# Kernel tuning notes

Measured on AMD Instinct MI355X. Metric: run time of the kernel, lower is better.

## Reference

```python
import jax, jax.numpy as jnp
import numpy as np

OUT_H = 7
OUT_W = 7
SPATIAL_SCALE = 0.25


def setup_inputs() -> dict:
    key = jax.random.key(0)
    k1, k2, k3, k4 = jax.random.split(key, 4)
    B, C, H, W = 2, 256, 256, 256
    N = 512  # rois per image
    x = jax.random.normal(k1, (B, C, H, W), dtype=jnp.float32)
    cxy = jax.random.uniform(k2, (B, N, 2), minval=0.0, maxval=1024.0, dtype=jnp.float32)
    wh = jax.random.uniform(k3, (B, N, 2), minval=16.0, maxval=256.0, dtype=jnp.float32)
    ang = jax.random.uniform(k4, (B, N, 1), minval=-90.0, maxval=90.0, dtype=jnp.float32)
    boxes = jnp.concatenate([cxy, wh, ang], axis=-1)  # [B, N, 5] = (cx, cy, w, h, angle_deg)
    return {"x": x, "boxes": boxes}


def _rroi_pool(feat, rois):
    # feat: [B, C, H, W]; rois: [R, 6] = (batch_idx, cx, cy, w, h, angle_deg)
    B, C, H, W = feat.shape
    R = rois.shape[0]
    b_idx = rois[:, 0].astype(jnp.int32)
    cx = rois[:, 1] * SPATIAL_SCALE
    cy = rois[:, 2] * SPATIAL_SCALE
    w = rois[:, 3] * SPATIAL_SCALE
    h = rois[:, 4] * SPATIAL_SCALE
    ang = rois[:, 5] * (jnp.pi / 180.0)
    # affine transform from bin-grid coords to (scaled) image coords (RRPN kernel)
    dx = -OUT_W / 2.0
    dy = -OUT_H / 2.0
    Sx = w / OUT_W
    Sy = h / OUT_H
    ca = jnp.cos(ang)
    sa = jnp.sin(ang)
    M00 = ca * Sx
    M01 = sa * Sy
    M02 = ca * Sx * dx + sa * Sy * dy + cx
    M10 = -sa * Sx
    M11 = ca * Sy
    M12 = -sa * Sx * dx + ca * Sy * dy + cy

    ph, pw = jnp.meshgrid(jnp.arange(OUT_H, dtype=jnp.float32),
                          jnp.arange(OUT_W, dtype=jnp.float32), indexing='ij')
    # 4 corners of each bin: offsets in (pw, ph)
    offs = jnp.array([[0.0, 0.0], [0.0, 1.0], [1.0, 0.0], [1.0, 1.0]], dtype=jnp.float32)
    pw_c = pw[None] + offs[:, 0][:, None, None]  # [4, OH, OW]
    ph_c = ph[None] + offs[:, 1][:, None, None]

    def aff(m0, m1, m2):
        # [R,1,1,1] * [4,OH,OW] -> [R,4,OH,OW]
        return (m0[:, None, None, None] * pw_c[None]
                + m1[:, None, None, None] * ph_c[None]
                + m2[:, None, None, None])

    Xc = aff(M00, M01, M02)  # x coords of bin corners
    Yc = aff(M10, M11, M12)
    leftMost = jnp.maximum(jnp.round(Xc.min(axis=1)), 0.0)            # [R,OH,OW]
    rightMost = jnp.minimum(jnp.round(Xc.max(axis=1)), W - 1.0)
    topMost = jnp.maximum(jnp.round(Yc.min(axis=1)), 0.0)
    bottomMost = jnp.minimum(jnp.round(Yc.max(axis=1)), H - 1.0)

    bin_cx = (leftMost + rightMost) / 2.0
    bin_cy = (topMost + bottomMost) / 2.0
    bin_l = jnp.floor(bin_cx).astype(jnp.int32)
    bin_r = jnp.ceil(bin_cx).astype(jnp.int32)
    bin_t = jnp.floor(bin_cy).astype(jnp.int32)
    bin_b = jnp.ceil(bin_cy).astype(jnp.int32)
    rx = bin_cx - jnp.floor(bin_cx)
    ry = bin_cy - jnp.floor(bin_cy)

    feat_t = feat.transpose(0, 2, 3, 1)  # [B, H, W, C]
    bi = b_idx[:, None, None]            # [R,1,1]

    def gather(yi, xi):
        valid = (yi >= 0) & (yi < H) & (xi >= 0) & (xi < W)
        yc = jnp.clip(yi, 0, H - 1)
        xc = jnp.clip(xi, 0, W - 1)
        v = feat_t[bi, yc, xc]                      # [R, OH, OW, C]
        return jnp.where(valid[..., None], v, 0.0)

    lt = gather(bin_t, bin_l)
    rt = gather(bin_t, bin_r)
    lb = gather(bin_b, bin_l)
    rb = gather(bin_b, bin_r)

    wlt = ((1.0 - rx) * (1.0 - ry))[..., None]
    wrt = (rx * (1.0 - ry))[..., None]
    wrb = (rx * ry)[..., None]
    wlb = ((1.0 - rx) * ry)[..., None]

    inter = lt * wlt + rt * wrt + rb * wrb + lb * wlb  # [R, OH, OW, C]
    out = jnp.maximum(inter, 0.0)  # kernel inits maxval=0 before the single sample
    return out.transpose(0, 3, 1, 2)  # [R, C, OH, OW]


def reference(x, boxes):
    # x: [B, C, H, W]; boxes: [B, N, 5]
    B, N = boxes.shape[0], boxes.shape[1]
    ids = jnp.repeat(jnp.arange(B, dtype=boxes.dtype), N)[:, None]  # convert_to_roi_format
    rois = jnp.concatenate([ids, boxes.reshape(B * N, 5)], axis=1)  # [R, 6]
    return _rroi_pool(x, rois)
```

## Files before the change

kernel.cpp:

```cpp
#include <hip/hip_runtime.h>

#define NBINS 49
#define NCH   256
#define FH    256
#define FW    256
#define HWSZ  (FH * FW)

typedef float f4 __attribute__((ext_vector_type(4)));

#define TD 64
__global__ __launch_bounds__(256) void transpose_chw_hwc(
    const float* __restrict__ in,
    float* __restrict__ outT)
{
    __shared__ float tile[TD][TD + 1];
    const int t   = threadIdx.x;
    const int hw0 = blockIdx.x * TD;
    const int c0  = blockIdx.y * TD;
    const int bz  = blockIdx.z;
    const float* A = in   + (size_t)bz * NCH * HWSZ;
    float*       B = outT + (size_t)bz * HWSZ * NCH;

    const int hwq = (t & 15) * 4;
    const int cr  = t >> 4;
    #pragma unroll
    for (int k = 0; k < 4; ++k) {
        int c = cr + k * 16;
        f4 v = __builtin_nontemporal_load(
                   (const f4*)&A[(size_t)(c0 + c) * HWSZ + hw0 + hwq]);
        tile[c][hwq + 0] = v.x;
        tile[c][hwq + 1] = v.y;
        tile[c][hwq + 2] = v.z;
        tile[c][hwq + 3] = v.w;
    }
    __syncthreads();
    const int cq  = (t & 15) * 4;
    const int hwr = t >> 4;
    #pragma unroll
    for (int k = 0; k < 4; ++k) {
        int hw = hwr + k * 16;
        f4 v;
        v.x = tile[cq + 0][hw];
        v.y = tile[cq + 1][hw];
        v.z = tile[cq + 2][hw];
        v.w = tile[cq + 3][hw];
        *(f4*)&B[(size_t)(hw0 + hw) * NCH + c0 + cq] = v;
    }
}

__global__ __launch_bounds__(256, 4) void rroi_pool_nhwc(
    const float* __restrict__ xt,
    const float* __restrict__ boxes,
    float* __restrict__ out)
{
    __shared__ int   s_oTL[NBINS], s_oTR[NBINS], s_oBL[NBINS], s_oBR[NBINS];
    __shared__ float s_wlt[NBINS], s_wrt[NBINS], s_wrb[NBINS], s_wlb[NBINS];
    __shared__ __align__(16) float s_stage[128 * NBINS];

    const int roi = blockIdx.x;
    const int tid = threadIdx.x;
    const int b   = roi >> 9;

    if (tid < NBINS) {
        const float* bx = boxes + roi * 5;
        float cx  = __fmul_rn(bx[0], 0.25f);
        float cy  = __fmul_rn(bx[1], 0.25f);
        float w   = __fmul_rn(bx[2], 0.25f);
        float h   = __fmul_rn(bx[3], 0.25f);
        float ang = __fmul_rn(bx[4], 0.017453292519943295f);
        float ca = (float)cos((double)ang);
        float sa = (float)sin((double)ang);
        float Sx = __fdiv_rn(w, 7.0f);
        float Sy = __fdiv_rn(h, 7.0f);
        const float dx = -3.5f, dy = -3.5f;
        float M00 = __fmul_rn(ca, Sx);
        float M01 = __fmul_rn(sa, Sy);
        float M02 = __fadd_rn(__fadd_rn(__fmul_rn(M00, dx), __fmul_rn(M01, dy)), cx);
        float nsa = -sa;
        float M10 = __fmul_rn(nsa, Sx);
        float M11 = __fmul_rn(ca, Sy);
        float M12 = __fadd_rn(__fadd_rn(__fmul_rn(M10, dx), __fmul_rn(M11, dy)), cy);

        int ph = tid / 7, pw = tid % 7;
        float minX = 1e30f, maxX = -1e30f, minY = 1e30f, maxY = -1e30f;
        #pragma unroll
        for (int o0 = 0; o0 < 2; ++o0) {
            #pragma unroll
            for (int o1 = 0; o1 < 2; ++o1) {
                float px = (float)(pw + o0);
                float py = (float)(ph + o1);
                float Xc = __fadd_rn(__fadd_rn(__fmul_rn(M00, px), __fmul_rn(M01, py)), M02);
                float Yc = __fadd_rn(__fadd_rn(__fmul_rn(M10, px), __fmul_rn(M11, py)), M12);
                minX = fminf(minX, Xc); maxX = fmaxf(maxX, Xc);
                minY = fminf(minY, Yc); maxY = fmaxf(maxY, Yc);
            }
        }
        float leftMost   = fmaxf(rintf(minX), 0.0f);
        float rightMost  = fminf(rintf(maxX), (float)(FW - 1));
        float topMost    = fmaxf(rintf(minY), 0.0f);
        float bottomMost = fminf(rintf(maxY), (float)(FH - 1));
        float bcx = __fmul_rn(__fadd_rn(leftMost, rightMost), 0.5f);
        float bcy = __fmul_rn(__fadd_rn(topMost, bottomMost), 0.5f);
        float fl = floorf(bcx), ft = floorf(bcy);
        int l   = (int)fl;
        int r   = (int)ceilf(bcx);
        int t   = (int)ft;
        int btm = (int)ceilf(bcy);
        float rx = __fsub_rn(bcx, fl);
        float ry = __fsub_rn(bcy, ft);

        bool vl = (unsigned)l   < (unsigned)FW;
        bool vr = (unsigned)r   < (unsigned)FW;
        bool vt = (unsigned)t   < (unsigned)FH;
        bool vb = (unsigned)btm < (unsigned)FH;
        int xl = min(max(l, 0), FW - 1), xr = min(max(r, 0), FW - 1);
        int yt = min(max(t, 0), FH - 1), yb = min(max(btm, 0), FH - 1);

        s_oTL[tid] = yt * FW + xl;
        s_oTR[tid] = yt * FW + xr;
        s_oBL[tid] = yb * FW + xl;
        s_oBR[tid] = yb * FW + xr;
        float w_lt = (1.0f - rx) * (1.0f - ry);
        float w_rt = rx * (1.0f - ry);
        float w_rb = rx * ry;
        float w_lb = (1.0f - rx) * ry;
        s_wlt[tid] = (vt && vl) ? w_lt : 0.0f;
        s_wrt[tid] = (vt && vr) ? w_rt : 0.0f;
        s_wrb[tid] = (vb && vr) ? w_rb : 0.0f;
        s_wlb[tid] = (vb && vl) ? w_lb : 0.0f;
    }
    __syncthreads();

    const float* fb = xt + (size_t)b * HWSZ * NCH;
    float p[NBINS];
    #pragma unroll
    for (int bin = 0; bin < NBINS; ++bin) {
        int oTL = __builtin_amdgcn_readfirstlane(s_oTL[bin]);
        int oTR = __builtin_amdgcn_readfirstlane(s_oTR[bin]);
        int oBL = __builtin_amdgcn_readfirstlane(s_oBL[bin]);
        int oBR = __builtin_amdgcn_readfirstlane(s_oBR[bin]);
        float wlt = s_wlt[bin], wrt = s_wrt[bin], wrb = s_wrb[bin], wlb = s_wlb[bin];
        float lt = fb[(size_t)oTL * NCH + tid];
        float rt = fb[(size_t)oTR * NCH + tid];
        float lb = fb[(size_t)oBL * NCH + tid];
        float rb = fb[(size_t)oBR * NCH + tid];
        float v = lt * wlt + rt * wrt + rb * wrb + lb * wlb;
        p[bin] = fmaxf(v, 0.0f);
    }

    f4* out4 = (f4*)(out + (size_t)roi * NCH * NBINS);
    const f4* lds4 = (const f4*)s_stage;
    const int HV4 = 128 * NBINS / 4;
    #pragma unroll
    for (int half = 0; half < 2; ++half) {
        __syncthreads();
        if ((tid >> 7) == half) {
            float* dst = s_stage + (tid & 127) * NBINS;
            #pragma unroll
            for (int bin = 0; bin < NBINS; ++bin) dst[bin] = p[bin];
        }
        __syncthreads();
        for (int j = tid; j < HV4; j += 256)
            __builtin_nontemporal_store(lds4[j], &out4[half * HV4 + j]);
    }
}

__global__ __launch_bounds__(256) void rroi_pool_chw(
    const float* __restrict__ x, const float* __restrict__ boxes, float* __restrict__ out)
{
    __shared__ int   s_l[NBINS], s_r[NBINS], s_t[NBINS], s_b[NBINS];
    __shared__ float s_rx[NBINS], s_ry[NBINS];
    const int roi = blockIdx.x, tid = threadIdx.x, b = roi >> 9;
    if (tid < NBINS) {
        const float* bx = boxes + roi * 5;
        float cx  = __fmul_rn(bx[0], 0.25f);
        float cy  = __fmul_rn(bx[1], 0.25f);
        float w   = __fmul_rn(bx[2], 0.25f);
        float h   = __fmul_rn(bx[3], 0.25f);
        float ang = __fmul_rn(bx[4], 0.017453292519943295f);
        float ca = (float)cos((double)ang);
        float sa = (float)sin((double)ang);
        float Sx = __fdiv_rn(w, 7.0f);
        float Sy = __fdiv_rn(h, 7.0f);
        const float dx = -3.5f, dy = -3.5f;
        float M00 = __fmul_rn(ca, Sx);
        float M01 = __fmul_rn(sa, Sy);
        float M02 = __fadd_rn(__fadd_rn(__fmul_rn(M00, dx), __fmul_rn(M01, dy)), cx);
        float nsa = -sa;
        float M10 = __fmul_rn(nsa, Sx);
        float M11 = __fmul_rn(ca, Sy);
        float M12 = __fadd_rn(__fadd_rn(__fmul_rn(M10, dx), __fmul_rn(M11, dy)), cy);
        int ph = tid / 7, pw = tid % 7;
        float minX = 1e30f, maxX = -1e30f, minY = 1e30f, maxY = -1e30f;
        #pragma unroll
        for (int o0 = 0; o0 < 2; ++o0)
            #pragma unroll
            for (int o1 = 0; o1 < 2; ++o1) {
                float px = (float)(pw + o0);
                float py = (float)(ph + o1);
                float Xc = __fadd_rn(__fadd_rn(__fmul_rn(M00, px), __fmul_rn(M01, py)), M02);
                float Yc = __fadd_rn(__fadd_rn(__fmul_rn(M10, px), __fmul_rn(M11, py)), M12);
                minX = fminf(minX, Xc); maxX = fmaxf(maxX, Xc);
                minY = fminf(minY, Yc); maxY = fmaxf(maxY, Yc);
            }
        float leftMost   = fmaxf(rintf(minX), 0.0f);
        float rightMost  = fminf(rintf(maxX), (float)(FW - 1));
        float topMost    = fmaxf(rintf(minY), 0.0f);
        float bottomMost = fminf(rintf(maxY), (float)(FH - 1));
        float bcx = __fmul_rn(__fadd_rn(leftMost, rightMost), 0.5f);
        float bcy = __fmul_rn(__fadd_rn(topMost, bottomMost), 0.5f);
        float fl = floorf(bcx), ft = floorf(bcy);
        s_l[tid] = (int)fl;  s_r[tid] = (int)ceilf(bcx);
        s_t[tid] = (int)ft;  s_b[tid] = (int)ceilf(bcy);
        s_rx[tid] = __fsub_rn(bcx, fl);
        s_ry[tid] = __fsub_rn(bcy, ft);
    }
    __syncthreads();
    const float* featb = x + (size_t)b * NCH * HWSZ;
    float* outr = out + (size_t)roi * NCH * NBINS;
    for (int i = tid; i < NCH * NBINS; i += 256) {
        int c = i / NBINS, bin = i - c * NBINS;
        int l = s_l[bin], r = s_r[bin], t = s_t[bin], btm = s_b[bin];
        float rx = s_rx[bin], ry = s_ry[bin];
        const float* fc = featb + (size_t)c * HWSZ;
        bool vl = (unsigned)l < (unsigned)FW, vr = (unsigned)r < (unsigned)FW;
        bool vt = (unsigned)t < (unsigned)FH, vb = (unsigned)btm < (unsigned)FH;
        int lc = min(max(l, 0), FW - 1), rc = min(max(r, 0), FW - 1);
        int tc = min(max(t, 0), FH - 1), bc = min(max(btm, 0), FH - 1);
        float lt = (vt && vl) ? fc[tc * FW + lc] : 0.0f;
        float rt = (vt && vr) ? fc[tc * FW + rc] : 0.0f;
        float lb = (vb && vl) ? fc[bc * FW + lc] : 0.0f;
        float rb = (vb && vr) ? fc[bc * FW + rc] : 0.0f;
        float w_lt = (1.0f - rx) * (1.0f - ry);
        float w_rt = rx * (1.0f - ry);
        float w_rb = rx * ry;
        float w_lb = (1.0f - rx) * ry;
        float v = lt * w_lt + rt * w_rt + rb * w_rb + lb * w_lb;
        outr[i] = fmaxf(v, 0.0f);
    }
}

extern "C" void kernel_launch(void* const* d_in, const int* in_sizes, int n_in,
                              void* d_out, int out_size, void* d_ws, size_t ws_size,
                              hipStream_t stream) {
    const float* x     = (const float*)d_in[0];
    const float* boxes = (const float*)d_in[1];
    float* out = (float*)d_out;
    (void)in_sizes; (void)n_in; (void)out_size;

    const size_t need = (size_t)2 * NCH * HWSZ * sizeof(float);
    if (ws_size >= need) {
        float* xt = (float*)d_ws;
        transpose_chw_hwc<<<dim3(HWSZ / TD, NCH / TD, 2), dim3(256), 0, stream>>>(x, xt);
        rroi_pool_nhwc<<<dim3(1024), dim3(256), 0, stream>>>(xt, boxes, out);
    } else {
        rroi_pool_chw<<<dim3(1024), dim3(256), 0, stream>>>(x, boxes, out);
    }
}
```

Measured before the change: 70.96 us.

## Transpose only feature pixels referenced by ROI bins via occupancy bitmap

Adds a pre-pass kernel that computes each ROI's bin sample corners and atomically sets bits in a per-batch pixel-occupancy bitmap. The CHW→HWC transpose then skips 64-pixel tiles with no referenced pixels and writes only the pixel rows that are marked. The goal is to cut the write traffic of the large transposed workspace, and part of the read traffic. The cost is an extra memset, a small bitmap kernel and its atomics, and duplicated bin geometry math.

After: 93.80 us. +32.2%, slower.

```diff
diff --git a/kernel.cpp b/kernel.cpp
--- a/kernel.cpp
+++ b/kernel.cpp
@@ -5,19 +5,116 @@
 #define FH    256
 #define FW    256
 #define HWSZ  (FH * FW)
+#define BMWORDS 2048
 
 typedef float f4 __attribute__((ext_vector_type(4)));
+
+__device__ __forceinline__ void bin_geom(const float* __restrict__ bx, int tid,
+                                         int& oTL, int& oTR, int& oBL, int& oBR,
+                                         float& wlt, float& wrt, float& wrb, float& wlb)
+{
+    float cx  = __fmul_rn(bx[0], 0.25f);
+    float cy  = __fmul_rn(bx[1], 0.25f);
+    float w   = __fmul_rn(bx[2], 0.25f);
+    float h   = __fmul_rn(bx[3], 0.25f);
+    float ang = __fmul_rn(bx[4], 0.017453292519943295f);
+    float ca = (float)cos((double)ang);
+    float sa = (float)sin((double)ang);
+    float Sx = __fdiv_rn(w, 7.0f);
+    float Sy = __fdiv_rn(h, 7.0f);
+    const float dx = -3.5f, dy = -3.5f;
+    float M00 = __fmul_rn(ca, Sx);
+    float M01 = __fmul_rn(sa, Sy);
+    float M02 = __fadd_rn(__fadd_rn(__fmul_rn(M00, dx), __fmul_rn(M01, dy)), cx);
+    float nsa = -sa;
+    float M10 = __fmul_rn(nsa, Sx);
+    float M11 = __fmul_rn(ca, Sy);
+    float M12 = __fadd_rn(__fadd_rn(__fmul_rn(M10, dx), __fmul_rn(M11, dy)), cy);
+
+    int ph = tid / 7, pw = tid % 7;
+    float minX = 1e30f, maxX = -1e30f, minY = 1e30f, maxY = -1e30f;
+    #pragma unroll
+    for (int o0 = 0; o0 < 2; ++o0) {
+        #pragma unroll
+        for (int o1 = 0; o1 < 2; ++o1) {
+            float px = (float)(pw + o0);
+            float py = (float)(ph + o1);
+            float Xc = __fadd_rn(__fadd_rn(__fmul_rn(M00, px), __fmul_rn(M01, py)), M02);
+            float Yc = __fadd_rn(__fadd_rn(__fmul_rn(M10, px), __fmul_rn(M11, py)), M12);
+            minX = fminf(minX, Xc); maxX = fmaxf(maxX, Xc);
+            minY = fminf(minY, Yc); maxY = fmaxf(maxY, Yc);
+        }
+    }
+    float leftMost   = fmaxf(rintf(minX), 0.0f);
+    float rightMost  = fminf(rintf(maxX), (float)(FW - 1));
+    float topMost    = fmaxf(rintf(minY), 0.0f);
+    float bottomMost = fminf(rintf(maxY), (float)(FH - 1));
+    float bcx = __fmul_rn(__fadd_rn(leftMost, rightMost), 0.5f);
+    float bcy = __fmul_rn(__fadd_rn(topMost, bottomMost), 0.5f);
+    float fl = floorf(bcx), ft = floorf(bcy);
+    int l   = (int)fl;
+    int r   = (int)ceilf(bcx);
+    int t   = (int)ft;
+    int btm = (int)ceilf(bcy);
+    float rx = __fsub_rn(bcx, fl);
+    float ry = __fsub_rn(bcy, ft);
+
+    bool vl = (unsigned)l   < (unsigned)FW;
+    bool vr = (unsigned)r   < (unsigned)FW;
+    bool vt = (unsigned)t   < (unsigned)FH;
+    bool vb = (unsigned)btm < (unsigned)FH;
+    int xl = min(max(l, 0), FW - 1), xr = min(max(r, 0), FW - 1);
+    int yt = min(max(t, 0), FH - 1), yb = min(max(btm, 0), FH - 1);
+
+    oTL = yt * FW + xl;
+    oTR = yt * FW + xr;
+    oBL = yb * FW + xl;
+    oBR = yb * FW + xr;
+    float w_lt = (1.0f - rx) * (1.0f - ry);
+    float w_rt = rx * (1.0f - ry);
+    float w_rb = rx * ry;
+    float w_lb = (1.0f - rx) * ry;
+    wlt = (vt && vl) ? w_lt : 0.0f;
+    wrt = (vt && vr) ? w_rt : 0.0f;
+    wrb = (vb && vr) ? w_rb : 0.0f;
+    wlb = (vb && vl) ? w_lb : 0.0f;
+}
+
+__global__ __launch_bounds__(64) void build_bitmap(
+    const float* __restrict__ boxes,
+    unsigned long long* __restrict__ bm)
+{
+    const int roi = blockIdx.x;
+    const int tid = threadIdx.x;
+    if (tid >= NBINS) return;
+    const int b = roi >> 9;
+    int oTL, oTR, oBL, oBR; float wlt, wrt, wrb, wlb;
+    bin_geom(boxes + roi * 5, tid, oTL, oTR, oBL, oBR, wlt, wrt, wrb, wlb);
+    unsigned long long* base = bm + (size_t)b * 1024;
+    atomicOr(&base[oTL >> 6], 1ull << (oTL & 63));
+    atomicOr(&base[oTR >> 6], 1ull << (oTR & 63));
+    atomicOr(&base[oBL >> 6], 1ull << (oBL & 63));
+    atomicOr(&base[oBR >> 6], 1ull << (oBR & 63));
+}
 
 #define TD 64
 __global__ __launch_bounds__(256) void transpose_chw_hwc(
     const float* __restrict__ in,
-    float* __restrict__ outT)
+    float* __restrict__ outT,
+    const unsigned long long* __restrict__ bm)
 {
     __shared__ float tile[TD][TD + 1];
     const int t   = threadIdx.x;
     const int hw0 = blockIdx.x * TD;
     const int c0  = blockIdx.y * TD;
     const int bz  = blockIdx.z;
+
+    unsigned long long mask = ~0ull;
+    if (bm) {
+        mask = bm[(size_t)bz * 1024 + blockIdx.x];
+        if (mask == 0ull) return;
+    }
+
     const float* A = in   + (size_t)bz * NCH * HWSZ;
     float*       B = outT + (size_t)bz * HWSZ * NCH;
 
@@ -39,12 +136,14 @@
     #pragma unroll
     for (int k = 0; k < 4; ++k) {
         int hw = hwr + k * 16;
-        f4 v;
-        v.x = tile[cq + 0][hw];
-        v.y = tile[cq + 1][hw];
-        v.z = tile[cq + 2][hw];
-        v.w = tile[cq + 3][hw];
-        *(f4*)&B[(size_t)(hw0 + hw) * NCH + c0 + cq] = v;
+        if ((mask >> hw) & 1ull) {
+            f4 v;
+            v.x = tile[cq + 0][hw];
+            v.y = tile[cq + 1][hw];
+            v.z = tile[cq + 2][hw];
+            v.w = tile[cq + 3][hw];
+            *(f4*)&B[(size_t)(hw0 + hw) * NCH + c0 + cq] = v;
+        }
     }
 }
 
@@ -62,72 +161,12 @@
     const int b   = roi >> 9;
 
     if (tid < NBINS) {
-        const float* bx = boxes + roi * 5;
-        float cx  = __fmul_rn(bx[0], 0.25f);
-        float cy  = __fmul_rn(bx[1], 0.25f);
-        float w   = __fmul_rn(bx[2], 0.25f);
-        float h   = __fmul_rn(bx[3], 0.25f);
-        float ang = __fmul_rn(bx[4], 0.017453292519943295f);
-        float ca = (float)cos((double)ang);
-        float sa = (float)sin((double)ang);
-        float Sx = __fdiv_rn(w, 7.0f);
-        float Sy = __fdiv_rn(h, 7.0f);
-        const float dx = -3.5f, dy = -3.5f;
-        float M00 = __fmul_rn(ca, Sx);
-        float M01 = __fmul_rn(sa, Sy);
-        float M02 = __fadd_rn(__fadd_rn(__fmul_rn(M00, dx), __fmul_rn(M01, dy)), cx);
-        float nsa = -sa;
-        float M10 = __fmul_rn(nsa, Sx);
-        float M11 = __fmul_rn(ca, Sy);
-        float M12 = __fadd_rn(__fadd_rn(__fmul_rn(M10, dx), __fmul_rn(M11, dy)), cy);
-
-        int ph = tid / 7, pw = tid % 7;
-        float minX = 1e30f, maxX = -1e30f, minY = 1e30f, maxY = -1e30f;
-        #pragma unroll
-        for (int o0 = 0; o0 < 2; ++o0) {
-            #pragma unroll
-            for (int o1 = 0; o1 < 2; ++o1) {
-                float px = (float)(pw + o0);
-                float py = (float)(ph + o1);
-                float Xc = __fadd_rn(__fadd_rn(__fmul_rn(M00, px), __fmul_rn(M01, py)), M02);
-                float Yc = __fadd_rn(__fadd_rn(__fmul_rn(M10, px), __fmul_rn(M11, py)), M12);
-                minX = fminf(minX, Xc); maxX = fmaxf(maxX, Xc);
-                minY = fminf(minY, Yc); maxY = fmaxf(maxY, Yc);
-            }
-        }
-        float leftMost   = fmaxf(rintf(minX), 0.0f);
-        float rightMost  = fminf(rintf(maxX), (float)(FW - 1));
-        float topMost    = fmaxf(rintf(minY), 0.0f);
-        float bottomMost = fminf(rintf(maxY), (float)(FH - 1));
-        float bcx = __fmul_rn(__fadd_rn(leftMost, rightMost), 0.5f);
-        float bcy = __fmul_rn(__fadd_rn(topMost, bottomMost), 0.5f);
-        float fl = floorf(bcx), ft = floorf(bcy);
-        int l   = (int)fl;
-        int r   = (int)ceilf(bcx);
-        int t   = (int)ft;
-        int btm = (int)ceilf(bcy);
-        float rx = __fsub_rn(bcx, fl);
-        float ry = __fsub_rn(bcy, ft);
-
-        bool vl = (unsigned)l   < (unsigned)FW;
-        bool vr = (unsigned)r   < (unsigned)FW;
-        bool vt = (unsigned)t   < (unsigned)FH;
-        bool vb = (unsigned)btm < (unsigned)FH;
-        int xl = min(max(l, 0), FW - 1), xr = min(max(r, 0), FW - 1);
-        int yt = min(max(t, 0), FH - 1), yb = min(max(btm, 0), FH - 1);
-
-        s_oTL[tid] = yt * FW + xl;
-        s_oTR[tid] = yt * FW + xr;
-        s_oBL[tid] = yb * FW + xl;
-        s_oBR[tid] = yb * FW + xr;
-        float w_lt = (1.0f - rx) * (1.0f - ry);
-        float w_rt = rx * (1.0f - ry);
-        float w_rb = rx * ry;
-        float w_lb = (1.0f - rx) * ry;
-        s_wlt[tid] = (vt && vl) ? w_lt : 0.0f;
-        s_wrt[tid] = (vt && vr) ? w_rt : 0.0f;
-        s_wrb[tid] = (vb && vr) ? w_rb : 0.0f;
-        s_wlb[tid] = (vb && vl) ? w_lb : 0.0f;
+        int oTL, oTR, oBL, oBR; float wlt, wrt, wrb, wlb;
+        bin_geom(boxes + roi * 5, tid, oTL, oTR, oBL, oBR, wlt, wrt, wrb, wlb);
+        s_oTL[tid] = oTL;  s_oTR[tid] = oTR;
+        s_oBL[tid] = oBL;  s_oBR[tid] = oBR;
+        s_wlt[tid] = wlt;  s_wrt[tid] = wrt;
+        s_wrb[tid] = wrb;  s_wlb[tid] = wlb;
     }
     __syncthreads();
 
@@ -248,10 +287,19 @@
     float* out = (float*)d_out;
     (void)in_sizes; (void)n_in; (void)out_size;
 
-    const size_t need = (size_t)2 * NCH * HWSZ * sizeof(float);
-    if (ws_size >= need) {
+    const size_t need_xt = (size_t)2 * NCH * HWSZ * sizeof(float);
+    const size_t need_bm = need_xt + BMWORDS * sizeof(unsigned long long);
+
+    if (ws_size >= need_bm) {
         float* xt = (float*)d_ws;
-        transpose_chw_hwc<<<dim3(HWSZ / TD, NCH / TD, 2), dim3(256), 0, stream>>>(x, xt);
+        unsigned long long* bm = (unsigned long long*)((char*)d_ws + need_xt);
+        hipMemsetAsync(bm, 0, BMWORDS * sizeof(unsigned long long), stream);
+        build_bitmap<<<dim3(1024), dim3(64), 0, stream>>>(boxes, bm);
+        transpose_chw_hwc<<<dim3(HWSZ / TD, NCH / TD, 2), dim3(256), 0, stream>>>(x, xt, bm);
+        rroi_pool_nhwc<<<dim3(1024), dim3(256), 0, stream>>>(xt, boxes, out);
+    } else if (ws_size >= need_xt) {
+        float* xt = (float*)d_ws;
+        transpose_chw_hwc<<<dim3(HWSZ / TD, NCH / TD, 2), dim3(256), 0, stream>>>(x, xt, nullptr);
         rroi_pool_nhwc<<<dim3(1024), dim3(256), 0, stream>>>(xt, boxes, out);
     } else {
         rroi_pool_chw<<<dim3(1024), dim3(256), 0, stream>>>(x, boxes, out);
```
